# Performance work log

Measured on AMD Instinct MI355X. Metric: run time of the kernel, lower is better.

The kernel has to match this reference:

```python
import jax, jax.numpy as jnp
import numpy as np

N, K, D = 8192, 256, 64

def setup_inputs() -> dict:
    key = jax.random.key(0)
    k1, k2, k3, k4, k5 = jax.random.split(key, 5)
    x = jax.random.normal(k1, (N, D), dtype=jnp.float32)
    means = 0.001 * jax.random.uniform(k2, (K, D), dtype=jnp.float32)
    diag = jax.random.normal(k3, (1, K, D), dtype=jnp.float32)
    tri = 0.01 * jax.random.normal(k4, (1, K, D, D), dtype=jnp.float32)
    weigh = jax.random.normal(k5, (1, K), dtype=jnp.float32)
    return {"x": x, "means": means, "diag": diag, "tri": tri, "weigh": weigh}

def reference(x, means, diag, tri, weigh):
    d = x.shape[1]
    logC = -d / 2 * jnp.log(jnp.asarray(2 * np.pi, dtype=x.dtype))
    w = jax.nn.log_softmax(weigh, axis=1)                 # [1,K]
    y = x[:, None, :] - means[None, :, :]                 # [N,K,d]
    lv = jnp.tanh(diag)                                   # [1,K,d]
    y = y * lv                                            # [N,K,d]
    L = jnp.tril(tri[0], k=-1)                            # [K,d,d] strictly lower
    y = y + jnp.einsum('kij,nkj->nki', L, y)              # [N,K,d]
    q = jnp.sum(y * y, axis=2)                            # [N,K]
    logdet = jnp.sum(jnp.log(jnp.abs(lv)), axis=2)        # [1,K]
    val = -q / 2 + logdet + w                             # [N,K]
    logpdf = logC + jax.nn.logsumexp(val, axis=-1)        # [N]
    return jnp.mean(-logpdf)                              # scalar
```

## Files before the change

### kernel.cpp

```cpp
#include <hip/hip_runtime.h>
#include <cstdint>
#include <cstddef>

#define NTOT 8192
#define KTOT 256

typedef _Float16 half2v __attribute__((ext_vector_type(2)));
typedef _Float16 half8  __attribute__((ext_vector_type(8)));
typedef float floatx16 __attribute__((ext_vector_type(16)));

static constexpr int    NJOBS   = 164;
static constexpr size_t G_ELEMS = (size_t)8 * NJOBS * 64 * 8;
static constexpr size_t OFF_CK  = G_ELEMS * 2;
static constexpr size_t OFF_CTR = OFF_CK + 1024;
static constexpr size_t OFF_VAL = OFF_CK + 4096;

__device__ __forceinline__ uint16_t f2h(float x) {
  _Float16 h = (_Float16)x;
  return __builtin_bit_cast(uint16_t, h);
}

__device__ __forceinline__ half8 mkh(half2v s, const half2v* rp) {
  union { half2v p[4]; half8 v; } u;
  u.p[0] = s * rp[0]; u.p[1] = s * rp[1]; u.p[2] = s * rp[2]; u.p[3] = s * rp[3];
  return u.v;
}
__device__ __forceinline__ half8 cph(const half2v* rp) {
  union { half2v p[4]; half8 v; } u;
  u.p[0] = rp[0]; u.p[1] = rp[1]; u.p[2] = rp[2]; u.p[3] = rp[3];
  return u.v;
}

__global__ void p1_prep(const float* __restrict__ means, const float* __restrict__ diag,
                        const float* __restrict__ tri, const float* __restrict__ weigh,
                        uint16_t* __restrict__ Gf, float* __restrict__ ck,
                        unsigned int* __restrict__ ctr, float* __restrict__ facc) {
  int k = blockIdx.x;
  int t = threadIdx.x;
  __shared__ float lv[64], ms[64], bv64[64], wred[256];
  __shared__ float Wp[64][68];
  __shared__ float SS[64][65];
  __shared__ float lse_s;

  if (k == 0 && t == 0) { *ctr = 0u; *facc = 0.f; }

  float wv = weigh[t];
  wred[t] = wv; __syncthreads();
  for (int o = 128; o > 0; o >>= 1) { if (t < o) wred[t] = fmaxf(wred[t], wred[t + o]); __syncthreads(); }
  float wm = wred[0]; __syncthreads();
  wred[t] = __expf(wv - wm); __syncthreads();
  for (int o = 128; o > 0; o >>= 1) { if (t < o) wred[t] += wred[t + o]; __syncthreads(); }
  if (t == 0) lse_s = wm + __logf(wred[0]);

  float logdet0 = 0.f;
  if (t < 64) {
    float d = diag[k * 64 + t];
    float l = tanhf(d);
    lv[t] = l;
    ms[t] = means[k * 64 + t];
    float ld = __logf(fabsf(l));
    #pragma unroll
    for (int o = 32; o > 0; o >>= 1) ld += __shfl_xor(ld, o);
    logdet0 = ld;
  }
  __syncthreads();

  for (int e = 0; e < 16; ++e) {
    int idx = e * 256 + t;
    int i = idx >> 6, c = idx & 63;
    float L = (c < i) ? tri[k * 4096 + idx] : 0.f;
    float w = ((c == i) ? 1.f : 0.f) + L;
    Wp[i][c] = w * lv[c];
  }
  __syncthreads();

  int i0 = (t >> 4) * 4, j0 = (t & 15) * 4;
  float acc[4][4];
  #pragma unroll
  for (int a = 0; a < 4; ++a)
    #pragma unroll
    for (int b = 0; b < 4; ++b) acc[a][b] = 0.f;
  for (int r = 0; r < 64; ++r) {
    float4 av = *(const float4*)&Wp[r][i0];
    float4 bv = *(const float4*)&Wp[r][j0];
    float aa[4] = {av.x, av.y, av.z, av.w};
    float bb[4] = {bv.x, bv.y, bv.z, bv.w};
    #pragma unroll
    for (int a = 0; a < 4; ++a)
      #pragma unroll
      for (int b = 0; b < 4; ++b) acc[a][b] = fmaf(aa[a], bb[b], acc[a][b]);
  }
  #pragma unroll
  for (int a = 0; a < 4; ++a)
    #pragma unroll
    for (int b = 0; b < 4; ++b) SS[i0 + a][j0 + b] = acc[a][b];
  __syncthreads();

  if (t < 64) {
    float b = 0.f;
    for (int j = 0; j < 64; ++j) b = fmaf(SS[t][j], ms[j], b);
    bv64[t] = b;
    float bm = b * ms[t];
    #pragma unroll
    for (int o = 32; o > 0; o >>= 1) bm += __shfl_xor(bm, o);
    if (t == 0) ck[k] = logdet0 + (weigh[k] - lse_s) - 0.5f * bm;
  }
  __syncthreads();

  int k32 = k >> 5, kl = k & 31;
  for (int hc = t; hc < 328; hc += 256) {
    float v[8];
    int job, half = hc & 1;
    if (hc < 320) {
      job = hc >> 1;
      int pp = job / 5, q = job - pp * 5;
      int i, c;
      if (pp < 16) { if (q < 4) { i = pp; c = q; } else { i = 63 - pp; c = 3; } }
      else         { if (q < 3) { i = pp; c = q + 1; } else { i = 63 - pp; c = q - 1; } }
      int jb = c * 16 + half * 8;
      #pragma unroll
      for (int e = 0; e < 8; ++e) {
        int j = jb + e;
        float s = SS[i][j];
        v[e] = (j < i) ? 0.f : ((j == i) ? -0.5f * s : -s);
      }
    } else {
      job = 160 + ((hc - 320) >> 1);
      int b0 = (hc - 320) * 8;
      #pragma unroll
      for (int e = 0; e < 8; ++e) v[e] = bv64[b0 + e];
    }
    uint4 pk;
    pk.x = (uint32_t)f2h(v[0]) | ((uint32_t)f2h(v[1]) << 16);
    pk.y = (uint32_t)f2h(v[2]) | ((uint32_t)f2h(v[3]) << 16);
    pk.z = (uint32_t)f2h(v[4]) | ((uint32_t)f2h(v[5]) << 16);
    pk.w = (uint32_t)f2h(v[6]) | ((uint32_t)f2h(v[7]) << 16);
    size_t base = ((size_t)(k32 * NJOBS + job) * 64 + half * 32 + kl) * 8;
    *(uint4*)(Gf + base) = pk;
  }
}

#define REFILL5(T0,T1,T2,T3,T4, jb) do {               \
    T0 = Bp[bofs + (size_t)((jb) + 0) * 64];           \
    T1 = Bp[bofs + (size_t)((jb) + 1) * 64];           \
    T2 = Bp[bofs + (size_t)((jb) + 2) * 64];           \
    T3 = Bp[bofs + (size_t)((jb) + 3) * 64];           \
    T4 = Bp[bofs + (size_t)((jb) + 4) * 64];           \
  } while (0)

#define MKY(pp)                                                             \
    float xa0f = xl[r0][(pp)],      xa1f = xl[r1][(pp)];                    \
    float xb0f = xl[r0][63 - (pp)], xb1f = xl[r1][63 - (pp)];               \
    _Float16 ha0 = (_Float16)xa0f; half2v ya0; ya0[0] = ha0; ya0[1] = ha0;  \
    _Float16 ha1 = (_Float16)xa1f; half2v ya1; ya1[0] = ha1; ya1[1] = ha1;  \
    _Float16 hb0 = (_Float16)xb0f; half2v yb0; yb0[0] = hb0; yb0[1] = hb0;  \
    _Float16 hb1 = (_Float16)xb1f; half2v yb1; yb1[0] = hb1; yb1[1] = hb1;

#define MM(AY0, AY1, RH, T) do {                                                          \
    half8 bb_ = __builtin_bit_cast(half8, T);                                             \
    acc0 = __builtin_amdgcn_mfma_f32_32x32x16_f16(mkh(AY0, runh0[RH]), bb_, acc0, 0,0,0); \
    acc1 = __builtin_amdgcn_mfma_f32_32x32x16_f16(mkh(AY1, runh1[RH]), bb_, acc1, 0,0,0); \
  } while (0)

#define CONSUME_A(pp, T0,T1,T2,T3,T4) do {  \
    MKY(pp)                                 \
    MM(ya0, ya1, 0, T0);                    \
    MM(ya0, ya1, 1, T1);                    \
    MM(ya0, ya1, 2, T2);                    \
    MM(ya0, ya1, 3, T3);                    \
    MM(yb0, yb1, 3, T4);                    \
  } while (0)

#define CONSUME_B(pp, T0,T1,T2,T3,T4) do {  \
    MKY(pp)                                 \
    MM(ya0, ya1, 1, T0);                    \
    MM(ya0, ya1, 2, T1);                    \
    MM(ya0, ya1, 3, T2);                    \
    MM(yb0, yb1, 2, T3);                    \
    MM(yb0, yb1, 3, T4);                    \
  } while (0)

__launch_bounds__(256)
__global__ void k2_gemm(const float* __restrict__ x, const uint16_t* __restrict__ Gf,
                        const float* __restrict__ ck, float* __restrict__ val2) {
  __shared__ float xl[128][65];
  int t = threadIdx.x;
  int bx = blockIdx.x, by = blockIdx.y;
  const float* xblk = x + (size_t)bx * (128 * 64);

  for (int e = 0; e < 8; ++e) {
    int lin = e * 1024 + t * 4;
    float4 v = *(const float4*)(xblk + lin);
    int r = lin >> 6, c = lin & 63;
    xl[r][c] = v.x; xl[r][c + 1] = v.y; xl[r][c + 2] = v.z; xl[r][c + 3] = v.w;
  }
  __syncthreads();

  int wave = t >> 6, l = t & 63;
  int wn = wave >> 1, wk = wave & 1;
  int half = l >> 5, lane31 = l & 31;
  int r0 = wn * 64 + lane31, r1 = r0 + 32;

  half2v runh0[4][4], runh1[4][4];
  #pragma unroll
  for (int c = 0; c < 4; ++c) {
    int base = c * 16 + half * 8;
    float4 ra = *(const float4*)(xblk + (size_t)r0 * 64 + base);
    float4 rb = *(const float4*)(xblk + (size_t)r0 * 64 + base + 4);
    runh0[c][0][0] = (_Float16)ra.x; runh0[c][0][1] = (_Float16)ra.y;
    runh0[c][1][0] = (_Float16)ra.z; runh0[c][1][1] = (_Float16)ra.w;
    runh0[c][2][0] = (_Float16)rb.x; runh0[c][2][1] = (_Float16)rb.y;
    runh0[c][3][0] = (_Float16)rb.z; runh0[c][3][1] = (_Float16)rb.w;
    float4 rc = *(const float4*)(xblk + (size_t)r1 * 64 + base);
    float4 rd = *(const float4*)(xblk + (size_t)r1 * 64 + base + 4);
    runh1[c][0][0] = (_Float16)rc.x; runh1[c][0][1] = (_Float16)rc.y;
    runh1[c][1][0] = (_Float16)rc.z; runh1[c][1][1] = (_Float16)rc.w;
    runh1[c][2][0] = (_Float16)rd.x; runh1[c][2][1] = (_Float16)rd.y;
    runh1[c][3][0] = (_Float16)rd.z; runh1[c][3][1] = (_Float16)rd.w;
  }

  int k32 = by * 2 + wk;
  const uint4* Bp = (const uint4*)Gf;
  size_t bofs = (size_t)(k32 * NJOBS) * 64 + l;

  floatx16 acc0, acc1;
  #pragma unroll
  for (int i = 0; i < 16; ++i) { acc0[i] = 0.f; acc1[i] = 0.f; }

  uint4 tA0, tA1, tA2, tA3, tA4, tB0, tB1, tB2, tB3, tB4;
  REFILL5(tA0, tA1, tA2, tA3, tA4, 0);
  REFILL5(tB0, tB1, tB2, tB3, tB4, 5);

  for (int pp = 0; pp < 16; pp += 2) {
    CONSUME_A(pp, tA0, tA1, tA2, tA3, tA4);
    REFILL5(tA0, tA1, tA2, tA3, tA4, (pp + 2) * 5);
    CONSUME_A(pp + 1, tB0, tB1, tB2, tB3, tB4);
    REFILL5(tB0, tB1, tB2, tB3, tB4, (pp + 3) * 5);
  }

  for (int pp = 16; pp < 30; pp += 2) {
    CONSUME_B(pp, tA0, tA1, tA2, tA3, tA4);
    REFILL5(tA0, tA1, tA2, tA3, tA4, (pp + 2) * 5);
    CONSUME_B(pp + 1, tB0, tB1, tB2, tB3, tB4);
    REFILL5(tB0, tB1, tB2, tB3, tB4, (pp + 3) * 5);
  }
  CONSUME_B(30, tA0, tA1, tA2, tA3, tA4);
  tA0 = Bp[bofs + (size_t)160 * 64];
  tA1 = Bp[bofs + (size_t)161 * 64];
  tA2 = Bp[bofs + (size_t)162 * 64];
  tA3 = Bp[bofs + (size_t)163 * 64];
  CONSUME_B(31, tB0, tB1, tB2, tB3, tB4);

  {
    half8 bb0 = __builtin_bit_cast(half8, tA0);
    acc0 = __builtin_amdgcn_mfma_f32_32x32x16_f16(cph(runh0[0]), bb0, acc0, 0, 0, 0);
    acc1 = __builtin_amdgcn_mfma_f32_32x32x16_f16(cph(runh1[0]), bb0, acc1, 0, 0, 0);
    half8 bb1 = __builtin_bit_cast(half8, tA1);
    acc0 = __builtin_amdgcn_mfma_f32_32x32x16_f16(cph(runh0[1]), bb1, acc0, 0, 0, 0);
    acc1 = __builtin_amdgcn_mfma_f32_32x32x16_f16(cph(runh1[1]), bb1, acc1, 0, 0, 0);
    half8 bb2 = __builtin_bit_cast(half8, tA2);
    acc0 = __builtin_amdgcn_mfma_f32_32x32x16_f16(cph(runh0[2]), bb2, acc0, 0, 0, 0);
    acc1 = __builtin_amdgcn_mfma_f32_32x32x16_f16(cph(runh1[2]), bb2, acc1, 0, 0, 0);
    half8 bb3 = __builtin_bit_cast(half8, tA3);
    acc0 = __builtin_amdgcn_mfma_f32_32x32x16_f16(cph(runh0[3]), bb3, acc0, 0, 0, 0);
    acc1 = __builtin_amdgcn_mfma_f32_32x32x16_f16(cph(runh1[3]), bb3, acc1, 0, 0, 0);
  }

  __syncthreads();
  float ckv = ck[by * 64 + wk * 32 + lane31];
  #pragma unroll
  for (int reg = 0; reg < 16; ++reg) {
    int row = (reg & 3) + 8 * (reg >> 2) + 4 * half;
    xl[wn * 64 + row][wk * 32 + lane31] = acc0[reg] + ckv;
    xl[wn * 64 + 32 + row][wk * 32 + lane31] = acc1[reg] + ckv;
  }
  __syncthreads();
  if (t < 128) {
    float m = -3.0e38f;
    #pragma unroll
    for (int j = 0; j < 64; ++j) m = fmaxf(m, xl[t][j]);
    float s = 0.f;
    #pragma unroll
    for (int j = 0; j < 64; ++j) s += __expf(xl[t][j] - m);
    size_t n = (size_t)bx * 128 + t;
    val2[n * 8 + by * 2 + 0] = m;
    val2[n * 8 + by * 2 + 1] = s;
  }
}

__global__ void k3_lse(const float* __restrict__ val2, float* __restrict__ facc,
                       unsigned int* __restrict__ ctr, float* __restrict__ out) {
  __shared__ float red[4];
  int t = threadIdx.x;
  size_t n = (size_t)blockIdx.x * 256 + t;
  const float4* p = (const float4*)(val2 + n * 8);
  float4 a = p[0], b = p[1];
  float M = fmaxf(fmaxf(a.x, a.z), fmaxf(b.x, b.z));
  float s = a.y * __expf(a.x - M) + a.w * __expf(a.z - M) +
            b.y * __expf(b.x - M) + b.w * __expf(b.z - M);
  float lse = M + __logf(s);
  #pragma unroll
  for (int o = 32; o > 0; o >>= 1) lse += __shfl_xor(lse, o);
  if ((t & 63) == 0) red[t >> 6] = lse;
  __syncthreads();
  if (t == 0) {
    float part = red[0] + red[1] + red[2] + red[3];
    atomicAdd(facc, part);
    __threadfence();
    unsigned int rank = atomicAdd(ctr, 1u);
    if (rank == 31) {
      float total = atomicAdd(facc, 0.0f);
      out[0] = 58.8120661251f - total / 8192.0f;
    }
  }
}

extern "C" void kernel_launch(void* const* d_in, const int* in_sizes, int n_in,
                              void* d_out, int out_size, void* d_ws, size_t ws_size,
                              hipStream_t stream) {
  const float* x     = (const float*)d_in[0];
  const float* means = (const float*)d_in[1];
  const float* diag  = (const float*)d_in[2];
  const float* tri   = (const float*)d_in[3];
  const float* weigh = (const float*)d_in[4];

  char* ws = (char*)d_ws;
  uint16_t* Gf       = (uint16_t*)ws;
  float* ck          = (float*)(ws + OFF_CK);
  unsigned int* ctr  = (unsigned int*)(ws + OFF_CTR);
  float* facc        = (float*)(ws + OFF_CTR + 4);
  float* val2        = (float*)(ws + OFF_VAL);

  p1_prep<<<dim3(256), dim3(256), 0, stream>>>(means, diag, tri, weigh, Gf, ck, ctr, facc);
  k2_gemm<<<dim3(64, 4), dim3(256), 0, stream>>>(x, Gf, ck, val2);
  k3_lse<<<dim3(32), dim3(256), 0, stream>>>(val2, facc, ctr, (float*)d_out);
}
```

Before: 92.99 us.

## Stage B fragments via direct global-to-LDS loads with per-wave double buffering

New measurement: 101.2 us. 8.8% more time.

```diff
diff --git a/kernel.cpp b/kernel.cpp
--- a/kernel.cpp
+++ b/kernel.cpp
@@ -8,6 +8,9 @@
 typedef _Float16 half2v __attribute__((ext_vector_type(2)));
 typedef _Float16 half8  __attribute__((ext_vector_type(8)));
 typedef float floatx16 __attribute__((ext_vector_type(16)));
+
+typedef __attribute__((address_space(3))) uint8_t        lds_b;
+typedef const __attribute__((address_space(1))) uint8_t  glb_b;
 
 static constexpr int    NJOBS   = 164;
 static constexpr size_t G_ELEMS = (size_t)8 * NJOBS * 64 * 8;
@@ -140,66 +143,58 @@
   }
 }
 
-#define REFILL5(T0,T1,T2,T3,T4, jb) do {               \
-    T0 = Bp[bofs + (size_t)((jb) + 0) * 64];           \
-    T1 = Bp[bofs + (size_t)((jb) + 1) * 64];           \
-    T2 = Bp[bofs + (size_t)((jb) + 2) * 64];           \
-    T3 = Bp[bofs + (size_t)((jb) + 3) * 64];           \
-    T4 = Bp[bofs + (size_t)((jb) + 4) * 64];           \
+#define MM2(AY0, AY1, RH, CH) do {                                                         \
+    half8 bb_ = __builtin_bit_cast(half8, CH);                                             \
+    acc0 = __builtin_amdgcn_mfma_f32_32x32x16_f16(mkh(AY0, runh0[RH]), bb_, acc0, 0,0,0);  \
+    acc1 = __builtin_amdgcn_mfma_f32_32x32x16_f16(mkh(AY1, runh1[RH]), bb_, acc1, 0,0,0);  \
   } while (0)
 
-#define MKY(pp)                                                             \
-    float xa0f = xl[r0][(pp)],      xa1f = xl[r1][(pp)];                    \
-    float xb0f = xl[r0][63 - (pp)], xb1f = xl[r1][63 - (pp)];               \
-    _Float16 ha0 = (_Float16)xa0f; half2v ya0; ya0[0] = ha0; ya0[1] = ha0;  \
-    _Float16 ha1 = (_Float16)xa1f; half2v ya1; ya1[0] = ha1; ya1[1] = ha1;  \
-    _Float16 hb0 = (_Float16)xb0f; half2v yb0; yb0[0] = hb0; yb0[1] = hb0;  \
-    _Float16 hb1 = (_Float16)xb1f; half2v yb1; yb1[0] = hb1; yb1[1] = hb1;
-
-#define MM(AY0, AY1, RH, T) do {                                                          \
-    half8 bb_ = __builtin_bit_cast(half8, T);                                             \
-    acc0 = __builtin_amdgcn_mfma_f32_32x32x16_f16(mkh(AY0, runh0[RH]), bb_, acc0, 0,0,0); \
-    acc1 = __builtin_amdgcn_mfma_f32_32x32x16_f16(mkh(AY1, runh1[RH]), bb_, acc1, 0,0,0); \
-  } while (0)
-
-#define CONSUME_A(pp, T0,T1,T2,T3,T4) do {  \
-    MKY(pp)                                 \
-    MM(ya0, ya1, 0, T0);                    \
-    MM(ya0, ya1, 1, T1);                    \
-    MM(ya0, ya1, 2, T2);                    \
-    MM(ya0, ya1, 3, T3);                    \
-    MM(yb0, yb1, 3, T4);                    \
-  } while (0)
-
-#define CONSUME_B(pp, T0,T1,T2,T3,T4) do {  \
-    MKY(pp)                                 \
-    MM(ya0, ya1, 1, T0);                    \
-    MM(ya0, ya1, 2, T1);                    \
-    MM(ya0, ya1, 3, T2);                    \
-    MM(yb0, yb1, 2, T3);                    \
-    MM(yb0, yb1, 3, T4);                    \
-  } while (0)
+static constexpr int    XLH_W     = 66;
+static constexpr size_t XLH_BYTES = (size_t)128 * XLH_W * 2;
+static constexpr int    STG_BUF   = 5120;
+static constexpr int    STG_WAVE  = 2 * STG_BUF;
 
 __launch_bounds__(256)
 __global__ void k2_gemm(const float* __restrict__ x, const uint16_t* __restrict__ Gf,
                         const float* __restrict__ ck, float* __restrict__ val2) {
-  __shared__ float xl[128][65];
+  __shared__ __align__(16) uint8_t smem[XLH_BYTES + 4 * STG_WAVE];
+  uint16_t* xl_h = (uint16_t*)smem;
   int t = threadIdx.x;
   int bx = blockIdx.x, by = blockIdx.y;
   const float* xblk = x + (size_t)bx * (128 * 64);
+
+  int wave = t >> 6, l = t & 63;
+  int wn = wave >> 1, wk = wave & 1;
+  int half = l >> 5, lane31 = l & 31;
+  int r0 = wn * 64 + lane31, r1 = r0 + 32;
+  int k32 = by * 2 + wk;
+
+  const uint8_t* GfB = (const uint8_t*)Gf;
+  size_t gbase = ((size_t)(k32 * NJOBS) * 64 + l) * 16;
+  uint8_t* stgw = smem + XLH_BYTES + wave * STG_WAVE;
+
+  auto STAGE = [&](int step, int buf) {
+    uint8_t* lb = stgw + buf * STG_BUF;
+    #pragma unroll
+    for (int c = 0; c < 5; ++c) {
+      int jc = (step < 32) ? (step * 5 + c) : ((c < 4) ? (160 + c) : 163);
+      __builtin_amdgcn_global_load_lds((glb_b*)(GfB + gbase + (size_t)jc * 1024),
+                                       (lds_b*)(lb + c * 1024), 16, 0, 0);
+    }
+  };
+
+  STAGE(0, 0);
+  STAGE(1, 1);
 
   for (int e = 0; e < 8; ++e) {
     int lin = e * 1024 + t * 4;
     float4 v = *(const float4*)(xblk + lin);
     int r = lin >> 6, c = lin & 63;
-    xl[r][c] = v.x; xl[r][c + 1] = v.y; xl[r][c + 2] = v.z; xl[r][c + 3] = v.w;
-  }
-  __syncthreads();
-
-  int wave = t >> 6, l = t & 63;
-  int wn = wave >> 1, wk = wave & 1;
-  int half = l >> 5, lane31 = l & 31;
-  int r0 = wn * 64 + lane31, r1 = r0 + 32;
+    uint32_t lo = (uint32_t)f2h(v.x) | ((uint32_t)f2h(v.y) << 16);
+    uint32_t hi = (uint32_t)f2h(v.z) | ((uint32_t)f2h(v.w) << 16);
+    uint32_t* p = (uint32_t*)&xl_h[r * XLH_W + c];
+    p[0] = lo; p[1] = hi;
+  }
 
   half2v runh0[4][4], runh1[4][4];
   #pragma unroll
@@ -218,70 +213,107 @@
     runh1[c][2][0] = (_Float16)rd.x; runh1[c][2][1] = (_Float16)rd.y;
     runh1[c][3][0] = (_Float16)rd.z; runh1[c][3][1] = (_Float16)rd.w;
   }
-
-  int k32 = by * 2 + wk;
-  const uint4* Bp = (const uint4*)Gf;
-  size_t bofs = (size_t)(k32 * NJOBS) * 64 + l;
+  __syncthreads();
 
   floatx16 acc0, acc1;
   #pragma unroll
   for (int i = 0; i < 16; ++i) { acc0[i] = 0.f; acc1[i] = 0.f; }
 
-  uint4 tA0, tA1, tA2, tA3, tA4, tB0, tB1, tB2, tB3, tB4;
-  REFILL5(tA0, tA1, tA2, tA3, tA4, 0);
-  REFILL5(tB0, tB1, tB2, tB3, tB4, 5);
-
-  for (int pp = 0; pp < 16; pp += 2) {
-    CONSUME_A(pp, tA0, tA1, tA2, tA3, tA4);
-    REFILL5(tA0, tA1, tA2, tA3, tA4, (pp + 2) * 5);
-    CONSUME_A(pp + 1, tB0, tB1, tB2, tB3, tB4);
-    REFILL5(tB0, tB1, tB2, tB3, tB4, (pp + 3) * 5);
-  }
-
-  for (int pp = 16; pp < 30; pp += 2) {
-    CONSUME_B(pp, tA0, tA1, tA2, tA3, tA4);
-    REFILL5(tA0, tA1, tA2, tA3, tA4, (pp + 2) * 5);
-    CONSUME_B(pp + 1, tB0, tB1, tB2, tB3, tB4);
-    REFILL5(tB0, tB1, tB2, tB3, tB4, (pp + 3) * 5);
-  }
-  CONSUME_B(30, tA0, tA1, tA2, tA3, tA4);
-  tA0 = Bp[bofs + (size_t)160 * 64];
-  tA1 = Bp[bofs + (size_t)161 * 64];
-  tA2 = Bp[bofs + (size_t)162 * 64];
-  tA3 = Bp[bofs + (size_t)163 * 64];
-  CONSUME_B(31, tB0, tB1, tB2, tB3, tB4);
+  for (int pp = 0; pp < 16; ++pp) {
+    const int cur = pp & 1;
+    const uint8_t* lb = stgw + cur * STG_BUF;
+    asm volatile("s_waitcnt vmcnt(5)" ::: "memory");
+    __builtin_amdgcn_sched_barrier(0);
+    _Float16 ha0 = __builtin_bit_cast(_Float16, xl_h[r0 * XLH_W + pp]);
+    _Float16 ha1 = __builtin_bit_cast(_Float16, xl_h[r1 * XLH_W + pp]);
+    _Float16 hb0 = __builtin_bit_cast(_Float16, xl_h[r0 * XLH_W + 63 - pp]);
+    _Float16 hb1 = __builtin_bit_cast(_Float16, xl_h[r1 * XLH_W + 63 - pp]);
+    half2v ya0; ya0[0] = ha0; ya0[1] = ha0;
+    half2v ya1; ya1[0] = ha1; ya1[1] = ha1;
+    half2v yb0; yb0[0] = hb0; yb0[1] = hb0;
+    half2v yb1; yb1[0] = hb1; yb1[1] = hb1;
+    uint4 c0 = *(const uint4*)(lb + 0 * 1024 + l * 16);
+    uint4 c1 = *(const uint4*)(lb + 1 * 1024 + l * 16);
+    uint4 c2 = *(const uint4*)(lb + 2 * 1024 + l * 16);
+    uint4 c3 = *(const uint4*)(lb + 3 * 1024 + l * 16);
+    uint4 c4 = *(const uint4*)(lb + 4 * 1024 + l * 16);
+    MM2(ya0, ya1, 0, c0);
+    MM2(ya0, ya1, 1, c1);
+    MM2(ya0, ya1, 2, c2);
+    MM2(ya0, ya1, 3, c3);
+    MM2(yb0, yb1, 3, c4);
+    asm volatile("s_waitcnt lgkmcnt(0)" ::: "memory");
+    __builtin_amdgcn_sched_barrier(0);
+    STAGE(pp + 2, cur);
+  }
+
+  for (int pp = 16; pp < 32; ++pp) {
+    const int cur = pp & 1;
+    const uint8_t* lb = stgw + cur * STG_BUF;
+    asm volatile("s_waitcnt vmcnt(5)" ::: "memory");
+    __builtin_amdgcn_sched_barrier(0);
+    _Float16 ha0 = __builtin_bit_cast(_Float16, xl_h[r0 * XLH_W + pp]);
+    _Float16 ha1 = __builtin_bit_cast(_Float16, xl_h[r1 * XLH_W + pp]);
+    _Float16 hb0 = __builtin_bit_cast(_Float16, xl_h[r0 * XLH_W + 63 - pp]);
+    _Float16 hb1 = __builtin_bit_cast(_Float16, xl_h[r1 * XLH_W + 63 - pp]);
+    half2v ya0; ya0[0] = ha0; ya0[1] = ha0;
+    half2v ya1; ya1[0] = ha1; ya1[1] = ha1;
+    half2v yb0; yb0[0] = hb0; yb0[1] = hb0;
+    half2v yb1; yb1[0] = hb1; yb1[1] = hb1;
+    uint4 c0 = *(const uint4*)(lb + 0 * 1024 + l * 16);
+    uint4 c1 = *(const uint4*)(lb + 1 * 1024 + l * 16);
+    uint4 c2 = *(const uint4*)(lb + 2 * 1024 + l * 16);
+    uint4 c3 = *(const uint4*)(lb + 3 * 1024 + l * 16);
+    uint4 c4 = *(const uint4*)(lb + 4 * 1024 + l * 16);
+    MM2(ya0, ya1, 1, c0);
+    MM2(ya0, ya1, 2, c1);
+    MM2(ya0, ya1, 3, c2);
+    MM2(yb0, yb1, 2, c3);
+    MM2(yb0, yb1, 3, c4);
+    asm volatile("s_waitcnt lgkmcnt(0)" ::: "memory");
+    __builtin_amdgcn_sched_barrier(0);
+    if (pp <= 30) STAGE(pp + 2, cur);
+  }
 
   {
-    half8 bb0 = __builtin_bit_cast(half8, tA0);
-    acc0 = __builtin_amdgcn_mfma_f32_32x32x16_f16(cph(runh0[0]), bb0, acc0, 0, 0, 0);
-    acc1 = __builtin_amdgcn_mfma_f32_32x32x16_f16(cph(runh1[0]), bb0, acc1, 0, 0, 0);
-    half8 bb1 = __builtin_bit_cast(half8, tA1);
-    acc0 = __builtin_amdgcn_mfma_f32_32x32x16_f16(cph(runh0[1]), bb1, acc0, 0, 0, 0);
-    acc1 = __builtin_amdgcn_mfma_f32_32x32x16_f16(cph(runh1[1]), bb1, acc1, 0, 0, 0);
-    half8 bb2 = __builtin_bit_cast(half8, tA2);
-    acc0 = __builtin_amdgcn_mfma_f32_32x32x16_f16(cph(runh0[2]), bb2, acc0, 0, 0, 0);
-    acc1 = __builtin_amdgcn_mfma_f32_32x32x16_f16(cph(runh1[2]), bb2, acc1, 0, 0, 0);
-    half8 bb3 = __builtin_bit_cast(half8, tA3);
-    acc0 = __builtin_amdgcn_mfma_f32_32x32x16_f16(cph(runh0[3]), bb3, acc0, 0, 0, 0);
-    acc1 = __builtin_amdgcn_mfma_f32_32x32x16_f16(cph(runh1[3]), bb3, acc1, 0, 0, 0);
-  }
-
-  __syncthreads();
+    const uint8_t* lb = stgw + 0 * STG_BUF;
+    asm volatile("s_waitcnt vmcnt(0)" ::: "memory");
+    __builtin_amdgcn_sched_barrier(0);
+    uint4 c0 = *(const uint4*)(lb + 0 * 1024 + l * 16);
+    uint4 c1 = *(const uint4*)(lb + 1 * 1024 + l * 16);
+    uint4 c2 = *(const uint4*)(lb + 2 * 1024 + l * 16);
+    uint4 c3 = *(const uint4*)(lb + 3 * 1024 + l * 16);
+    half8 b0 = __builtin_bit_cast(half8, c0);
+    acc0 = __builtin_amdgcn_mfma_f32_32x32x16_f16(cph(runh0[0]), b0, acc0, 0, 0, 0);
+    acc1 = __builtin_amdgcn_mfma_f32_32x32x16_f16(cph(runh1[0]), b0, acc1, 0, 0, 0);
+    half8 b1 = __builtin_bit_cast(half8, c1);
+    acc0 = __builtin_amdgcn_mfma_f32_32x32x16_f16(cph(runh0[1]), b1, acc0, 0, 0, 0);
+    acc1 = __builtin_amdgcn_mfma_f32_32x32x16_f16(cph(runh1[1]), b1, acc1, 0, 0, 0);
+    half8 b2 = __builtin_bit_cast(half8, c2);
+    acc0 = __builtin_amdgcn_mfma_f32_32x32x16_f16(cph(runh0[2]), b2, acc0, 0, 0, 0);
+    acc1 = __builtin_amdgcn_mfma_f32_32x32x16_f16(cph(runh1[2]), b2, acc1, 0, 0, 0);
+    half8 b3 = __builtin_bit_cast(half8, c3);
+    acc0 = __builtin_amdgcn_mfma_f32_32x32x16_f16(cph(runh0[3]), b3, acc0, 0, 0, 0);
+    acc1 = __builtin_amdgcn_mfma_f32_32x32x16_f16(cph(runh1[3]), b3, acc1, 0, 0, 0);
+  }
+
+  __syncthreads();
+  float* vals = (float*)(smem + XLH_BYTES);
   float ckv = ck[by * 64 + wk * 32 + lane31];
   #pragma unroll
   for (int reg = 0; reg < 16; ++reg) {
     int row = (reg & 3) + 8 * (reg >> 2) + 4 * half;
-    xl[wn * 64 + row][wk * 32 + lane31] = acc0[reg] + ckv;
-    xl[wn * 64 + 32 + row][wk * 32 + lane31] = acc1[reg] + ckv;
+    vals[(wn * 64 + row) * 65 + wk * 32 + lane31] = acc0[reg] + ckv;
+    vals[(wn * 64 + 32 + row) * 65 + wk * 32 + lane31] = acc1[reg] + ckv;
   }
   __syncthreads();
   if (t < 128) {
     float m = -3.0e38f;
     #pragma unroll
-    for (int j = 0; j < 64; ++j) m = fmaxf(m, xl[t][j]);
+    for (int j = 0; j < 64; ++j) m = fmaxf(m, vals[t * 65 + j]);
     float s = 0.f;
     #pragma unroll
-    for (int j = 0; j < 64; ++j) s += __expf(xl[t][j] - m);
+    for (int j = 0; j < 64; ++j) s += __expf(vals[t * 65 + j] - m);
     size_t n = (size_t)bx * 128 + t;
     val2[n * 8 + by * 2 + 0] = m;
     val2[n * 8 + by * 2 + 1] = s;
```

## Split GEMM rows across eight waves with one accumulator each

Applied to the files above, without the earlier changes.

Measured after the change: 94.21 us. About the same (+1.3%).

```diff
diff --git a/kernel.cpp b/kernel.cpp
--- a/kernel.cpp
+++ b/kernel.cpp
@@ -149,38 +149,35 @@
   } while (0)
 
 #define MKY(pp)                                                             \
-    float xa0f = xl[r0][(pp)],      xa1f = xl[r1][(pp)];                    \
-    float xb0f = xl[r0][63 - (pp)], xb1f = xl[r1][63 - (pp)];               \
-    _Float16 ha0 = (_Float16)xa0f; half2v ya0; ya0[0] = ha0; ya0[1] = ha0;  \
-    _Float16 ha1 = (_Float16)xa1f; half2v ya1; ya1[0] = ha1; ya1[1] = ha1;  \
-    _Float16 hb0 = (_Float16)xb0f; half2v yb0; yb0[0] = hb0; yb0[1] = hb0;  \
-    _Float16 hb1 = (_Float16)xb1f; half2v yb1; yb1[0] = hb1; yb1[1] = hb1;
-
-#define MM(AY0, AY1, RH, T) do {                                                          \
-    half8 bb_ = __builtin_bit_cast(half8, T);                                             \
-    acc0 = __builtin_amdgcn_mfma_f32_32x32x16_f16(mkh(AY0, runh0[RH]), bb_, acc0, 0,0,0); \
-    acc1 = __builtin_amdgcn_mfma_f32_32x32x16_f16(mkh(AY1, runh1[RH]), bb_, acc1, 0,0,0); \
+    _Float16 ha = (_Float16)xl[r][(pp)];                                    \
+    _Float16 hb = (_Float16)xl[r][63 - (pp)];                               \
+    half2v ya; ya[0] = ha; ya[1] = ha;                                      \
+    half2v yb; yb[0] = hb; yb[1] = hb;
+
+#define MM1(AY, RH, T) do {                                                              \
+    half8 bb_ = __builtin_bit_cast(half8, T);                                            \
+    acc = __builtin_amdgcn_mfma_f32_32x32x16_f16(mkh(AY, runh[RH]), bb_, acc, 0,0,0);    \
   } while (0)
 
 #define CONSUME_A(pp, T0,T1,T2,T3,T4) do {  \
     MKY(pp)                                 \
-    MM(ya0, ya1, 0, T0);                    \
-    MM(ya0, ya1, 1, T1);                    \
-    MM(ya0, ya1, 2, T2);                    \
-    MM(ya0, ya1, 3, T3);                    \
-    MM(yb0, yb1, 3, T4);                    \
+    MM1(ya, 0, T0);                         \
+    MM1(ya, 1, T1);                         \
+    MM1(ya, 2, T2);                         \
+    MM1(ya, 3, T3);                         \
+    MM1(yb, 3, T4);                         \
   } while (0)
 
 #define CONSUME_B(pp, T0,T1,T2,T3,T4) do {  \
     MKY(pp)                                 \
-    MM(ya0, ya1, 1, T0);                    \
-    MM(ya0, ya1, 2, T1);                    \
-    MM(ya0, ya1, 3, T2);                    \
-    MM(yb0, yb1, 2, T3);                    \
-    MM(yb0, yb1, 3, T4);                    \
+    MM1(ya, 1, T0);                         \
+    MM1(ya, 2, T1);                         \
+    MM1(ya, 3, T2);                         \
+    MM1(yb, 2, T3);                         \
+    MM1(yb, 3, T4);                         \
   } while (0)
 
-__launch_bounds__(256)
+__launch_bounds__(512)
 __global__ void k2_gemm(const float* __restrict__ x, const uint16_t* __restrict__ Gf,
                         const float* __restrict__ ck, float* __restrict__ val2) {
   __shared__ float xl[128][65];
@@ -188,8 +185,8 @@
   int bx = blockIdx.x, by = blockIdx.y;
   const float* xblk = x + (size_t)bx * (128 * 64);
 
-  for (int e = 0; e < 8; ++e) {
-    int lin = e * 1024 + t * 4;
+  for (int e = 0; e < 4; ++e) {
+    int lin = e * 2048 + t * 4;
     float4 v = *(const float4*)(xblk + lin);
     int r = lin >> 6, c = lin & 63;
     xl[r][c] = v.x; xl[r][c + 1] = v.y; xl[r][c + 2] = v.z; xl[r][c + 3] = v.w;
@@ -199,33 +196,27 @@
   int wave = t >> 6, l = t & 63;
   int wn = wave >> 1, wk = wave & 1;
   int half = l >> 5, lane31 = l & 31;
-  int r0 = wn * 64 + lane31, r1 = r0 + 32;
-
-  half2v runh0[4][4], runh1[4][4];
+  int r = wn * 32 + lane31;
+
+  half2v runh[4][4];
   #pragma unroll
   for (int c = 0; c < 4; ++c) {
     int base = c * 16 + half * 8;
-    float4 ra = *(const float4*)(xblk + (size_t)r0 * 64 + base);
-    float4 rb = *(const float4*)(xblk + (size_t)r0 * 64 + base + 4);
-    runh0[c][0][0] = (_Float16)ra.x; runh0[c][0][1] = (_Float16)ra.y;
-    runh0[c][1][0] = (_Float16)ra.z; runh0[c][1][1] = (_Float16)ra.w;
-    runh0[c][2][0] = (_Float16)rb.x; runh0[c][2][1] = (_Float16)rb.y;
-    runh0[c][3][0] = (_Float16)rb.z; runh0[c][3][1] = (_Float16)rb.w;
-    float4 rc = *(const float4*)(xblk + (size_t)r1 * 64 + base);
-    float4 rd = *(const float4*)(xblk + (size_t)r1 * 64 + base + 4);
-    runh1[c][0][0] = (_Float16)rc.x; runh1[c][0][1] = (_Float16)rc.y;
-    runh1[c][1][0] = (_Float16)rc.z; runh1[c][1][1] = (_Float16)rc.w;
-    runh1[c][2][0] = (_Float16)rd.x; runh1[c][2][1] = (_Float16)rd.y;
-    runh1[c][3][0] = (_Float16)rd.z; runh1[c][3][1] = (_Float16)rd.w;
+    float4 ra = *(const float4*)(xblk + (size_t)r * 64 + base);
+    float4 rb = *(const float4*)(xblk + (size_t)r * 64 + base + 4);
+    runh[c][0][0] = (_Float16)ra.x; runh[c][0][1] = (_Float16)ra.y;
+    runh[c][1][0] = (_Float16)ra.z; runh[c][1][1] = (_Float16)ra.w;
+    runh[c][2][0] = (_Float16)rb.x; runh[c][2][1] = (_Float16)rb.y;
+    runh[c][3][0] = (_Float16)rb.z; runh[c][3][1] = (_Float16)rb.w;
   }
 
   int k32 = by * 2 + wk;
   const uint4* Bp = (const uint4*)Gf;
   size_t bofs = (size_t)(k32 * NJOBS) * 64 + l;
 
-  floatx16 acc0, acc1;
-  #pragma unroll
-  for (int i = 0; i < 16; ++i) { acc0[i] = 0.f; acc1[i] = 0.f; }
+  floatx16 acc;
+  #pragma unroll
+  for (int i = 0; i < 16; ++i) acc[i] = 0.f;
 
   uint4 tA0, tA1, tA2, tA3, tA4, tB0, tB1, tB2, tB3, tB4;
   REFILL5(tA0, tA1, tA2, tA3, tA4, 0);
@@ -253,17 +244,13 @@
 
   {
     half8 bb0 = __builtin_bit_cast(half8, tA0);
-    acc0 = __builtin_amdgcn_mfma_f32_32x32x16_f16(cph(runh0[0]), bb0, acc0, 0, 0, 0);
-    acc1 = __builtin_amdgcn_mfma_f32_32x32x16_f16(cph(runh1[0]), bb0, acc1, 0, 0, 0);
+    acc = __builtin_amdgcn_mfma_f32_32x32x16_f16(cph(runh[0]), bb0, acc, 0, 0, 0);
     half8 bb1 = __builtin_bit_cast(half8, tA1);
-    acc0 = __builtin_amdgcn_mfma_f32_32x32x16_f16(cph(runh0[1]), bb1, acc0, 0, 0, 0);
-    acc1 = __builtin_amdgcn_mfma_f32_32x32x16_f16(cph(runh1[1]), bb1, acc1, 0, 0, 0);
+    acc = __builtin_amdgcn_mfma_f32_32x32x16_f16(cph(runh[1]), bb1, acc, 0, 0, 0);
     half8 bb2 = __builtin_bit_cast(half8, tA2);
-    acc0 = __builtin_amdgcn_mfma_f32_32x32x16_f16(cph(runh0[2]), bb2, acc0, 0, 0, 0);
-    acc1 = __builtin_amdgcn_mfma_f32_32x32x16_f16(cph(runh1[2]), bb2, acc1, 0, 0, 0);
+    acc = __builtin_amdgcn_mfma_f32_32x32x16_f16(cph(runh[2]), bb2, acc, 0, 0, 0);
     half8 bb3 = __builtin_bit_cast(half8, tA3);
-    acc0 = __builtin_amdgcn_mfma_f32_32x32x16_f16(cph(runh0[3]), bb3, acc0, 0, 0, 0);
-    acc1 = __builtin_amdgcn_mfma_f32_32x32x16_f16(cph(runh1[3]), bb3, acc1, 0, 0, 0);
+    acc = __builtin_amdgcn_mfma_f32_32x32x16_f16(cph(runh[3]), bb3, acc, 0, 0, 0);
   }
 
   __syncthreads();
@@ -271,8 +258,7 @@
   #pragma unroll
   for (int reg = 0; reg < 16; ++reg) {
     int row = (reg & 3) + 8 * (reg >> 2) + 4 * half;
-    xl[wn * 64 + row][wk * 32 + lane31] = acc0[reg] + ckv;
-    xl[wn * 64 + 32 + row][wk * 32 + lane31] = acc1[reg] + ckv;
+    xl[wn * 32 + row][wk * 32 + lane31] = acc[reg] + ckv;
   }
   __syncthreads();
   if (t < 128) {
@@ -332,6 +318,6 @@
   float* val2        = (float*)(ws + OFF_VAL);
 
   p1_prep<<<dim3(256), dim3(256), 0, stream>>>(means, diag, tri, weigh, Gf, ck, ctr, facc);
-  k2_gemm<<<dim3(64, 4), dim3(256), 0, stream>>>(x, Gf, ck, val2);
+  k2_gemm<<<dim3(64, 4), dim3(512), 0, stream>>>(x, Gf, ck, val2);
   k3_lse<<<dim3(32), dim3(256), 0, stream>>>(val2, facc, ctr, (float*)d_out);
 }
```
